# Optimization experiments

Hardware: AMD Instinct MI355X
Metric: run time of the kernel (lower is better)

Reference implementation:

```python
import jax, jax.numpy as jnp
import numpy as np

NUM_HEADS = 16
PAD_ID = 0.0  # max(config.pad_id, 0)


def setup_inputs() -> dict:
    key = jax.random.key(0)
    ks = jax.random.split(key, 9)
    B, T, C = 2, 2048, 1024
    x = jax.random.normal(ks[0], (B, T, C), dtype=jnp.float32)
    # xavier_uniform-like scale for square [C, C] weights
    lim = (6.0 / (C + C)) ** 0.5
    def w(k):
        return jax.random.uniform(k, (C, C), dtype=jnp.float32, minval=-lim, maxval=lim)
    def b(k):
        return jax.random.uniform(k, (C,), dtype=jnp.float32)  # nn.init.uniform_ default [0,1)
    return {
        "x": x,
        "wq_w": w(ks[1]), "wq_b": b(ks[2]),
        "wk_w": w(ks[3]), "wk_b": b(ks[4]),
        "wv_w": w(ks[5]), "wv_b": b(ks[6]),
        "wo_w": w(ks[7]), "wo_b": b(ks[8]),
    }


def reference(x, wq_w, wq_b, wk_w, wk_b, wv_w, wv_b, wo_w, wo_b):
    B, T, C = x.shape
    H = NUM_HEADS
    Dh = C // H
    scale = Dh ** -0.5

    # Linear layers (torch Linear: x @ W.T + b), then split heads -> [B, T, H, Dh]
    q = (x @ wq_w.T + wq_b).reshape(B, T, H, Dh)
    k = (x @ wk_w.T + wk_b).reshape(B, T, H, Dh)
    v = (x @ wv_w.T + wv_b).reshape(B, T, H, Dh)

    # scores: [B, H, Tq, Tk]
    scores = jnp.einsum("bthd,bshd->bhts", q, k) * scale

    # Padding mask over keys: (x[:,:,0] != pad_id) -> [B, 1, 1, Tk]
    key_mask = (x[:, :, 0] != PAD_ID)[:, None, None, :]
    scores = jnp.where(key_mask, scores, -jnp.inf)

    attn = jax.nn.softmax(scores, axis=-1)

    out = jnp.einsum("bhts,bshd->bthd", attn, v).reshape(B, T, C)
    return out @ wo_w.T + wo_b
```

## Files before the change

### kernel.cpp

```cpp
#include <hip/hip_runtime.h>
#include <hip/hip_bf16.h>

typedef short short8 __attribute__((ext_vector_type(8)));
typedef float f32x4 __attribute__((ext_vector_type(4)));

#define MFMA32(a, b, c) __builtin_amdgcn_mfma_f32_16x16x32_bf16(a, b, c, 0, 0, 0)

#if __has_builtin(__builtin_amdgcn_exp2f)
#define EXP2F(x) __builtin_amdgcn_exp2f(x)
#else
#define EXP2F(x) exp2f(x)
#endif

#define GLL16(gp, lp) __builtin_amdgcn_global_load_lds(                                  \
    (__attribute__((address_space(1))) unsigned int*)(unsigned long long)(const void*)(gp), \
    (__attribute__((address_space(3))) unsigned int*)(lp), 16, 0, 0)

__device__ __forceinline__ unsigned short f2b(float f) {
    union { float f; unsigned int u; } v;
    v.f = f;
    unsigned int u = v.u;
    return (unsigned short)((u + 0x7fffu + ((u >> 16) & 1u)) >> 16);
}

static __device__ __forceinline__ f32x4 max4(f32x4 x, f32x4 y) {
    f32x4 r;
    r[0] = fmaxf(x[0], y[0]); r[1] = fmaxf(x[1], y[1]);
    r[2] = fmaxf(x[2], y[2]); r[3] = fmaxf(x[3], y[3]);
    return r;
}

__global__ void cvt_all(const float* __restrict__ x,
                        const float* __restrict__ w0, const float* __restrict__ w1,
                        const float* __restrict__ w2, const float* __restrict__ w3,
                        unsigned short* __restrict__ xb, unsigned short* __restrict__ wb,
                        float* __restrict__ maskbuf) {
    int blk = blockIdx.x;
    if (blk < 4096) {
        int i = blk * 256 + threadIdx.x;
        float4 v = ((const float4*)x)[i];
        ushort4 o;
        o.x = f2b(v.x); o.y = f2b(v.y); o.z = f2b(v.z); o.w = f2b(v.w);
        ((ushort4*)xb)[i] = o;
        if ((i & 255) == 0)
            maskbuf[i >> 8] = (v.x != 0.0f) ? 0.0f : -1e30f;
    } else {
        int wi = blk - 4096;
        int widx = wi >> 10;
        int i = (wi & 1023) * 256 + threadIdx.x;
        const float* src = widx == 0 ? w0 : (widx == 1 ? w1 : (widx == 2 ? w2 : w3));
        float4 v = ((const float4*)src)[i];
        ushort4 o;
        o.x = f2b(v.x); o.y = f2b(v.y); o.z = f2b(v.z); o.w = f2b(v.w);
        ((ushort4*)(wb + ((size_t)widx << 20)))[i] = o;
    }
}

#define QSCALE (0.125f * 1.44269504088896341f)

__global__ __launch_bounds__(256) void gemm_qkv(
        const unsigned short* __restrict__ A,
        const unsigned short* __restrict__ wq, const unsigned short* __restrict__ wk,
        const unsigned short* __restrict__ wv,
        const float* __restrict__ bq, const float* __restrict__ bk,
        const float* __restrict__ bv,
        unsigned short* __restrict__ qbuf, unsigned short* __restrict__ kbuf,
        unsigned short* __restrict__ vbuf) {
    __shared__ __attribute__((aligned(16))) unsigned short As[2][128 * 32];
    __shared__ __attribute__((aligned(16))) unsigned short Bs[2][128 * 32];
    int tid = threadIdx.x;
    int lane = tid & 63, wave = tid >> 6;
    int lane15 = lane & 15, quad = lane >> 4;
    int seg = blockIdx.x >> 3;
    int bn = (blockIdx.x & 7) * 128;
    int bm = blockIdx.y * 128;
    const unsigned short* Bw = seg == 0 ? wq : (seg == 1 ? wk : wv);
    const float* bias = seg == 0 ? bq : (seg == 1 ? bk : bv);
    int wm = (wave >> 1) * 64, wn = (wave & 1) * 64;

    f32x4 acc[4][4];
#pragma unroll
    for (int i = 0; i < 4; i++)
#pragma unroll
        for (int j = 0; j < 4; j++) acc[i][j] = (f32x4){0.f, 0.f, 0.f, 0.f};

    int arow = tid >> 2, acol = (tid & 3) * 8;
    const unsigned short* A0 = &A[(size_t)(bm + arow) * 1024 + acol];
    const unsigned short* A1 = A0 + (size_t)64 * 1024;
    const unsigned short* B0 = &Bw[(size_t)(bn + arow) * 1024 + acol];
    const unsigned short* B1 = B0 + (size_t)64 * 1024;

    GLL16(A0, &As[0][(size_t)tid * 8]);
    GLL16(A1, &As[0][(size_t)(tid + 256) * 8]);
    GLL16(B0, &Bs[0][(size_t)tid * 8]);
    GLL16(B1, &Bs[0][(size_t)(tid + 256) * 8]);

    for (int it = 0; it < 32; it++) {
        int cur = it & 1;
        __syncthreads();
        if (it < 31) {
            int kn = (it + 1) * 32;
            GLL16(A0 + kn, &As[cur ^ 1][(size_t)tid * 8]);
            GLL16(A1 + kn, &As[cur ^ 1][(size_t)(tid + 256) * 8]);
            GLL16(B0 + kn, &Bs[cur ^ 1][(size_t)tid * 8]);
            GLL16(B1 + kn, &Bs[cur ^ 1][(size_t)(tid + 256) * 8]);
        }
        const unsigned short* as = As[cur];
        const unsigned short* bs = Bs[cur];
        short8 af[4], bf[4];
#pragma unroll
        for (int i = 0; i < 4; i++)
            af[i] = *(const short8*)&as[(wm + i * 16 + lane15) * 32 + quad * 8];
#pragma unroll
        for (int j = 0; j < 4; j++)
            bf[j] = *(const short8*)&bs[(wn + j * 16 + lane15) * 32 + quad * 8];
#pragma unroll
        for (int i = 0; i < 4; i++)
#pragma unroll
            for (int j = 0; j < 4; j++)
                acc[i][j] = MFMA32(af[i], bf[j], acc[i][j]);
    }

    int bb = bm >> 11;
#pragma unroll
    for (int j = 0; j < 4; j++) {
        int nl = bn + wn + j * 16 + lane15;
        int h = nl >> 6, d = nl & 63;
        float bv_ = bias[nl];
        if (seg == 2) {
            size_t vbase = ((size_t)((bb * 16 + h) * 64 + d)) * 2048;
#pragma unroll
            for (int i = 0; i < 4; i++) {
                int tk0 = (bm & 2047) + wm + i * 16 + quad * 4;
                int grp = tk0 >> 5;
                ushort4 pk;
                pk.x = f2b(acc[i][j][0] + bv_);
                pk.y = f2b(acc[i][j][1] + bv_);
                pk.z = f2b(acc[i][j][2] + bv_);
                pk.w = f2b(acc[i][j][3] + bv_);
                *(ushort4*)&vbuf[vbase + grp * 32 + quad * 8 + (i & 1) * 4] = pk;
            }
        } else {
#pragma unroll
            for (int i = 0; i < 4; i++)
#pragma unroll
                for (int r = 0; r < 4; r++) {
                    int m = bm + wm + i * 16 + quad * 4 + r;
                    int tk = m & 2047;
                    float v = acc[i][j][r] + bv_;
                    size_t off = ((size_t)((bb * 16 + h) * 2048 + tk)) * 64 + d;
                    if (seg == 0) qbuf[off] = f2b(v * QSCALE);
                    else          kbuf[off] = f2b(v);
                }
        }
    }
}

__global__ __launch_bounds__(256) void gemm_proj(
        const unsigned short* __restrict__ A, const unsigned short* __restrict__ Bw,
        const float* __restrict__ bias, float* __restrict__ out) {
    __shared__ __attribute__((aligned(16))) unsigned short As[2][64 * 32];
    __shared__ __attribute__((aligned(16))) unsigned short Bs[2][128 * 32];
    int tid = threadIdx.x;
    int lane = tid & 63, wave = tid >> 6;
    int lane15 = lane & 15, quad = lane >> 4;
    int bn = blockIdx.x * 128, bm = blockIdx.y * 64;
    int wm = (wave >> 1) * 32, wn = (wave & 1) * 64;

    f32x4 acc[2][4];
#pragma unroll
    for (int i = 0; i < 2; i++)
#pragma unroll
        for (int j = 0; j < 4; j++) acc[i][j] = (f32x4){0.f, 0.f, 0.f, 0.f};

    int arow = tid >> 2, acol = (tid & 3) * 8;
    const unsigned short* A0 = &A[(size_t)(bm + arow) * 1024 + acol];
    const unsigned short* B0 = &Bw[(size_t)(bn + arow) * 1024 + acol];
    const unsigned short* B1 = B0 + (size_t)64 * 1024;

    GLL16(A0, &As[0][(size_t)tid * 8]);
    GLL16(B0, &Bs[0][(size_t)tid * 8]);
    GLL16(B1, &Bs[0][(size_t)(tid + 256) * 8]);

    for (int it = 0; it < 32; it++) {
        int cur = it & 1;
        __syncthreads();
        if (it < 31) {
            int kn = (it + 1) * 32;
            GLL16(A0 + kn, &As[cur ^ 1][(size_t)tid * 8]);
            GLL16(B0 + kn, &Bs[cur ^ 1][(size_t)tid * 8]);
            GLL16(B1 + kn, &Bs[cur ^ 1][(size_t)(tid + 256) * 8]);
        }
        const unsigned short* as = As[cur];
        const unsigned short* bs = Bs[cur];
        short8 af[2], bf[4];
#pragma unroll
        for (int i = 0; i < 2; i++)
            af[i] = *(const short8*)&as[(wm + i * 16 + lane15) * 32 + quad * 8];
#pragma unroll
        for (int j = 0; j < 4; j++)
            bf[j] = *(const short8*)&bs[(wn + j * 16 + lane15) * 32 + quad * 8];
#pragma unroll
        for (int i = 0; i < 2; i++)
#pragma unroll
            for (int j = 0; j < 4; j++)
                acc[i][j] = MFMA32(af[i], bf[j], acc[i][j]);
    }

#pragma unroll
    for (int j = 0; j < 4; j++) {
        int n = bn + wn + j * 16 + lane15;
        float bv_ = bias[n];
#pragma unroll
        for (int i = 0; i < 2; i++)
#pragma unroll
            for (int r = 0; r < 4; r++) {
                int m = bm + wm + i * 16 + quad * 4 + r;
                out[(size_t)m * 1024 + n] = acc[i][j][r] + bv_;
            }
    }
}

__global__ __launch_bounds__(512, 4) void attn_kernel(
        const unsigned short* __restrict__ qbuf, const unsigned short* __restrict__ kbuf,
        const unsigned short* __restrict__ vtbuf, const float* __restrict__ maskbuf,
        unsigned short* __restrict__ attnout) {
    __shared__ __attribute__((aligned(16))) unsigned short Ks[2][128 * 64];
    __shared__ __attribute__((aligned(16))) unsigned short Vs[2][64 * 128];

    int id = blockIdx.x;
    int combo = (id & 7) | (((id >> 7) & 3) << 3);
    int qt = (id >> 3) & 15;
    int b = combo >> 4, h = combo & 15;
    int tid = threadIdx.x, lane = tid & 63, wave = tid >> 6;
    int lane15 = lane & 15, quad = lane >> 4;
    int q0 = qt * 128 + wave * 16;

    const unsigned short* Q  = qbuf  + (size_t)combo * 2048 * 64;
    const unsigned short* Kp = kbuf  + (size_t)combo * 2048 * 64;
    const unsigned short* Vt = vtbuf + (size_t)combo * 64 * 2048;
    const float* mb = maskbuf + b * 2048;

    short8 qf[2];
#pragma unroll
    for (int g = 0; g < 2; g++)
        qf[g] = *(const short8*)&Q[(size_t)(q0 + lane15) * 64 + g * 32 + quad * 8];

    float m_run = -1e30f, l_run = 0.f;
    f32x4 o[4];
#pragma unroll
    for (int c = 0; c < 4; c++) o[c] = (f32x4){0.f, 0.f, 0.f, 0.f};

    const f32x4 z4 = {0.f, 0.f, 0.f, 0.f};
    int x7 = lane15 & 7;
    int ci0 = tid;

#pragma unroll
    for (int r2 = 0; r2 < 2; r2++) {
        int ci = ci0 + r2 * 512;
        int kr = ci >> 3, kc = (ci & 7) ^ (kr & 7);
        GLL16(&Kp[(size_t)kr * 64 + kc * 8], &Ks[0][(size_t)ci * 8]);
        int vd = ci >> 4, vc = (ci & 15) ^ (vd & 15);
        GLL16(&Vt[(size_t)vd * 2048 + vc * 8], &Vs[0][(size_t)ci * 8]);
    }

    for (int it = 0; it < 16; it++) {
        int cur = it & 1;
        int kb = it * 128;
        __syncthreads();
        if (it < 15) {
            int kn = kb + 128;
#pragma unroll
            for (int r2 = 0; r2 < 2; r2++) {
                int ci = ci0 + r2 * 512;
                int kr = ci >> 3, kc = (ci & 7) ^ (kr & 7);
                GLL16(&Kp[(size_t)(kn + kr) * 64 + kc * 8], &Ks[cur ^ 1][(size_t)ci * 8]);
                int vd = ci >> 4, vc = (ci & 15) ^ (vd & 15);
                GLL16(&Vt[(size_t)vd * 2048 + kn + vc * 8], &Vs[cur ^ 1][(size_t)ci * 8]);
            }
        }
        const unsigned short* ks = Ks[cur];
        const unsigned short* vs = Vs[cur];

        f32x4 s[8];
#pragma unroll
        for (int t = 0; t < 8; t++) {
            int row = t * 16 + lane15;
            short8 k0 = *(const short8*)&ks[row * 64 + (quad ^ x7) * 8];
            short8 k1 = *(const short8*)&ks[row * 64 + ((quad + 4) ^ x7) * 8];
            f32x4 t0 = MFMA32(k0, qf[0], z4);
            s[t] = MFMA32(k1, qf[1], t0);
        }
#pragma unroll
        for (int t = 0; t < 8; t++)
            s[t] += *(const f32x4*)&mb[kb + t * 16 + quad * 4];

        f32x4 m4 = s[0];
#pragma unroll
        for (int t = 1; t < 8; t++) m4 = max4(m4, s[t]);
        float mx = fmaxf(fmaxf(m4[0], m4[1]), fmaxf(m4[2], m4[3]));
        mx = fmaxf(mx, __shfl_xor(mx, 16));
        mx = fmaxf(mx, __shfl_xor(mx, 32));
        float mnew = fmaxf(m_run, mx);
        float alpha = EXP2F(m_run - mnew);
        m_run = mnew;
        float ls = 0.f;
        short8 pb8[4];
#pragma unroll
        for (int g = 0; g < 4; g++) {
            float e0 = EXP2F(s[2 * g][0] - mnew);
            float e1 = EXP2F(s[2 * g][1] - mnew);
            float e2 = EXP2F(s[2 * g][2] - mnew);
            float e3 = EXP2F(s[2 * g][3] - mnew);
            float f0 = EXP2F(s[2 * g + 1][0] - mnew);
            float f1 = EXP2F(s[2 * g + 1][1] - mnew);
            float f2 = EXP2F(s[2 * g + 1][2] - mnew);
            float f3 = EXP2F(s[2 * g + 1][3] - mnew);
            ls += ((e0 + e1) + (e2 + e3)) + ((f0 + f1) + (f2 + f3));
            union { uint4 u; short8 sv; } pu;
            pu.u.x = __builtin_amdgcn_perm(__float_as_uint(e1), __float_as_uint(e0), 0x07060302u);
            pu.u.y = __builtin_amdgcn_perm(__float_as_uint(e3), __float_as_uint(e2), 0x07060302u);
            pu.u.z = __builtin_amdgcn_perm(__float_as_uint(f1), __float_as_uint(f0), 0x07060302u);
            pu.u.w = __builtin_amdgcn_perm(__float_as_uint(f3), __float_as_uint(f2), 0x07060302u);
            pb8[g] = pu.sv;
        }
        l_run = l_run * alpha + ls;
#pragma unroll
        for (int c = 0; c < 4; c++) o[c] *= alpha;

#pragma unroll
        for (int c = 0; c < 4; c++) {
            int d = c * 16 + lane15;
#pragma unroll
            for (int g = 0; g < 4; g++) {
                int skc = (g * 4 + quad) ^ lane15;
                short8 vv = *(const short8*)&vs[d * 128 + skc * 8];
                o[c] = MFMA32(vv, pb8[g], o[c]);
            }
        }
    }

    float l = l_run;
    l += __shfl_xor(l, 16);
    l += __shfl_xor(l, 32);
    float rl = 1.0f / l;
    size_t row = (size_t)(b * 2048 + q0 + lane15) * 1024 + h * 64 + quad * 4;
#pragma unroll
    for (int c = 0; c < 4; c++) {
        ushort4 pk;
        pk.x = f2b(o[c][0] * rl);
        pk.y = f2b(o[c][1] * rl);
        pk.z = f2b(o[c][2] * rl);
        pk.w = f2b(o[c][3] * rl);
        *(ushort4*)&attnout[row + c * 16] = pk;
    }
}

extern "C" void kernel_launch(void* const* d_in, const int* in_sizes, int n_in,
                              void* d_out, int out_size, void* d_ws, size_t ws_size,
                              hipStream_t stream) {
    const float* x    = (const float*)d_in[0];
    const float* wq_w = (const float*)d_in[1];
    const float* wq_b = (const float*)d_in[2];
    const float* wk_w = (const float*)d_in[3];
    const float* wk_b = (const float*)d_in[4];
    const float* wv_w = (const float*)d_in[5];
    const float* wv_b = (const float*)d_in[6];
    const float* wo_w = (const float*)d_in[7];
    const float* wo_b = (const float*)d_in[8];
    float* out = (float*)d_out;

    char* ws = (char*)d_ws;
    size_t off = 0;
    unsigned short* xb      = (unsigned short*)(ws + off); off += (size_t)4096 * 1024 * 2;
    unsigned short* wb      = (unsigned short*)(ws + off); off += (size_t)4 * 1024 * 1024 * 2;
    unsigned short* qbuf    = (unsigned short*)(ws + off); off += (size_t)4096 * 1024 * 2;
    unsigned short* kbuf    = (unsigned short*)(ws + off); off += (size_t)4096 * 1024 * 2;
    unsigned short* vbuf    = (unsigned short*)(ws + off); off += (size_t)4096 * 1024 * 2;
    unsigned short* attnout = (unsigned short*)(ws + off); off += (size_t)4096 * 1024 * 2;
    float* maskbuf          = (float*)(ws + off);          off += 4096 * 4;

    unsigned short* wqb = wb;
    unsigned short* wkb = wb + (1u << 20);
    unsigned short* wvb = wb + (2u << 20);
    unsigned short* wob = wb + (3u << 20);

    cvt_all<<<8192, 256, 0, stream>>>(x, wq_w, wk_w, wv_w, wo_w, xb, wb, maskbuf);

    gemm_qkv<<<dim3(24, 32), 256, 0, stream>>>(xb, wqb, wkb, wvb,
                                               wq_b, wk_b, wv_b, qbuf, kbuf, vbuf);

    attn_kernel<<<512, 512, 0, stream>>>(qbuf, kbuf, vbuf, maskbuf, attnout);

    gemm_proj<<<dim3(8, 64), 256, 0, stream>>>(attnout, wob, wo_b, out);
}
```

Before: 213.7 us.

## Load V fragments directly from global memory instead of staging in LDS

Removes the double-buffered LDS staging of the transposed V tile. Each lane now reads its V MFMA operands straight from global memory in two batches, with the first batch issued before the softmax to hide latency. This halves LDS use, which may allow more resident blocks, and removes the LDS write/read traffic for V. In exchange, V reads are no longer shared across the 8 waves of a block, so global/L2 traffic for V rises up to eightfold and load latency is exposed inside the loop.

```diff
diff --git a/kernel.cpp b/kernel.cpp
--- a/kernel.cpp
+++ b/kernel.cpp
@@ -226,7 +226,6 @@
         const unsigned short* __restrict__ vtbuf, const float* __restrict__ maskbuf,
         unsigned short* __restrict__ attnout) {
     __shared__ __attribute__((aligned(16))) unsigned short Ks[2][128 * 64];
-    __shared__ __attribute__((aligned(16))) unsigned short Vs[2][64 * 128];
 
     int id = blockIdx.x;
     int combo = (id & 7) | (((id >> 7) & 3) << 3);
@@ -255,13 +254,13 @@
     int x7 = lane15 & 7;
     int ci0 = tid;
 
+    const unsigned short* Vrow = &Vt[(size_t)lane15 * 2048 + quad * 8];
+
 #pragma unroll
     for (int r2 = 0; r2 < 2; r2++) {
         int ci = ci0 + r2 * 512;
         int kr = ci >> 3, kc = (ci & 7) ^ (kr & 7);
         GLL16(&Kp[(size_t)kr * 64 + kc * 8], &Ks[0][(size_t)ci * 8]);
-        int vd = ci >> 4, vc = (ci & 15) ^ (vd & 15);
-        GLL16(&Vt[(size_t)vd * 2048 + vc * 8], &Vs[0][(size_t)ci * 8]);
     }
 
     for (int it = 0; it < 16; it++) {
@@ -275,12 +274,9 @@
                 int ci = ci0 + r2 * 512;
                 int kr = ci >> 3, kc = (ci & 7) ^ (kr & 7);
                 GLL16(&Kp[(size_t)(kn + kr) * 64 + kc * 8], &Ks[cur ^ 1][(size_t)ci * 8]);
-                int vd = ci >> 4, vc = (ci & 15) ^ (vd & 15);
-                GLL16(&Vt[(size_t)vd * 2048 + kn + vc * 8], &Vs[cur ^ 1][(size_t)ci * 8]);
             }
         }
         const unsigned short* ks = Ks[cur];
-        const unsigned short* vs = Vs[cur];
 
         f32x4 s[8];
 #pragma unroll
@@ -291,6 +287,14 @@
             f32x4 t0 = MFMA32(k0, qf[0], z4);
             s[t] = MFMA32(k1, qf[1], t0);
         }
+
+        short8 vf01[2][4];
+#pragma unroll
+        for (int c = 0; c < 2; c++)
+#pragma unroll
+            for (int g = 0; g < 4; g++)
+                vf01[c][g] = *(const short8*)(Vrow + (size_t)c * 16 * 2048 + kb + g * 32);
+
 #pragma unroll
         for (int t = 0; t < 8; t++)
             s[t] += *(const f32x4*)&mb[kb + t * 16 + quad * 4];
@@ -328,16 +332,23 @@
 #pragma unroll
         for (int c = 0; c < 4; c++) o[c] *= alpha;
 
-#pragma unroll
-        for (int c = 0; c < 4; c++) {
-            int d = c * 16 + lane15;
-#pragma unroll
-            for (int g = 0; g < 4; g++) {
-                int skc = (g * 4 + quad) ^ lane15;
-                short8 vv = *(const short8*)&vs[d * 128 + skc * 8];
-                o[c] = MFMA32(vv, pb8[g], o[c]);
-            }
-        }
+        short8 vf23[2][4];
+#pragma unroll
+        for (int c = 0; c < 2; c++)
+#pragma unroll
+            for (int g = 0; g < 4; g++)
+                vf23[c][g] = *(const short8*)(Vrow + (size_t)(c + 2) * 16 * 2048 + kb + g * 32);
+
+#pragma unroll
+        for (int c = 0; c < 2; c++)
+#pragma unroll
+            for (int g = 0; g < 4; g++)
+                o[c] = MFMA32(vf01[c][g], pb8[g], o[c]);
+#pragma unroll
+        for (int c = 0; c < 2; c++)
+#pragma unroll
+            for (int g = 0; g < 4; g++)
+                o[c + 2] = MFMA32(vf23[c][g], pb8[g], o[c + 2]);
     }
 
     float l = l_run;
```

Result: slower. 282.9 us (+32.4%).
